# Kernel tuning notes

Measured on AMD Instinct MI355X. Metric: run time of the kernel, lower is better.

The kernel has to match this reference:

```python
import jax, jax.numpy as jnp
import numpy as np

N, C, H, W = 8, 128, 56, 56
CO = C // 8  # 16


def setup_inputs() -> dict:
    key = jax.random.key(0)
    k1, k2, k3, k4 = jax.random.split(key, 4)
    x = jax.random.normal(k1, (N, C, H, W), dtype=jnp.float32)
    # p_3: Conv2d(c*35 -> c//8, 1x1). The unfold channel order is (c, kh=5, kw=7),
    # so the 1x1 conv over c*35 channels is exactly a dilated 5x7 conv with
    # weight [CO, C, 5, 7] and rhs_dilation (2, 3).
    w3 = jax.random.normal(k2, (CO, C, 5, 7), dtype=jnp.float32) * 0.02
    w4 = jax.random.normal(k3, (CO, CO), dtype=jnp.float32) * 0.1
    w5 = jax.random.normal(k4, (C, CO), dtype=jnp.float32) * 0.1
    return {"x": x, "w3": w3, "w4": w4, "w5": w5}


def reference(x, w3, w4, w5):
    # Fused equivalent of: unfold(5x1, dil 2, pad 4) -> unfold(1x7, dil 3, pad 9)
    # -> 1x1 conv (c*35 -> c//8). Padding (4,4)/(9,9) keeps 'same' spatial size.
    y = jax.lax.conv_general_dilated(
        x, w3,
        window_strides=(1, 1),
        padding=((4, 4), (9, 9)),
        rhs_dilation=(2, 3),
        dimension_numbers=("NCHW", "OIHW", "NCHW"),
    )  # [N, CO, H, W]
    y = jnp.einsum("oc,nchw->nohw", w4, y)  # p_4: 1x1 conv CO->CO
    y = jnp.einsum("oc,nchw->nohw", w5, y)  # p_5: 1x1 conv CO->C
    return y
```

## Files before the change

### kernel.cpp

```cpp
#include <hip/hip_runtime.h>

#define BN 8
#define BC 128
#define BH 56
#define BW 56
#define HW 3136
#define NTAP 35
#define WS_WC 71680
#define WS_XP (WS_WC + 4096)
#define XROW 2368
#define XS_OFF 0
#define Y3_OFF 15360
#define WA_OFF 17920
#define SMEM_SZ 53760

typedef unsigned short u16;
typedef unsigned int u32;
typedef __bf16 bf16x8 __attribute__((ext_vector_type(8)));
typedef float f32x4 __attribute__((ext_vector_type(4)));

__device__ __forceinline__ u16 f2b(float f) {
    unsigned u = __float_as_uint(f);
    return (u16)((u + 0x7FFFu + ((u >> 16) & 1u)) >> 16);
}
__device__ __forceinline__ u32 pack2(float a, float b) {
    return (u32)f2b(a) | ((u32)f2b(b) << 16);
}
__device__ __forceinline__ void dma16(const void* g, void* l) {
    __builtin_amdgcn_global_load_lds(
        (const __attribute__((address_space(1))) u32*)g,
        (__attribute__((address_space(3))) u32*)l, 16, 0, 0);
}

__global__ __launch_bounds__(256) void prep_all(
    const float* __restrict__ x, const float* __restrict__ w3,
    const float* __restrict__ w4, const float* __restrict__ w5,
    u16* __restrict__ ws)
{
    const int b = blockIdx.x;
    const int tid = threadIdx.x;

    if (b >= 2048) {
        int i = (b - 2048) * 256 + tid;
        if (i < WS_WC) {
            int j = i & 7, lane = (i >> 3) & 63, r = i >> 9;
            int tap = r % NTAP, cc = r / NTAP;
            int q = lane >> 4, lm = lane & 15;
            ws[i] = f2b(w3[(lm * BC + cc * 32 + q * 8 + j) * NTAP + tap]);
        } else if (i < WS_WC + 4096) {
            int i2 = i - WS_WC;
            int j = i2 & 7, lane = (i2 >> 3) & 63, ot = i2 >> 9;
            int q = lane >> 4, lm = lane & 15, o = ot * 16 + lm, k = q * 8 + j;
            float s = 0.f;
            if (k < 16)
                for (int c = 0; c < 16; ++c) s += w5[o * 16 + c] * w4[c * 16 + k];
            ws[i] = f2b(s);
        }
        return;
    }

    __shared__ float ls[32][57];
    const int hp = b & 63, cc = (b >> 6) & 3, n = b >> 8;
    u32* dst = (u32*)(ws + WS_XP + (size_t)((n * 4 + cc) * 64 + hp) * XROW);
    const int gr = hp - 4;

    if ((unsigned)gr >= BH) {
        for (int i = tid; i < XROW / 2; i += 256) dst[i] = 0u;
        return;
    }
    for (int i = tid; i < 32 * 14; i += 256) {
        int c = i / 14, w4i = i % 14;
        float4 v = *(const float4*)(x + ((size_t)(n * BC + cc * 32 + c) * BH + gr) * BW + 4 * w4i);
        ls[c][4 * w4i + 0] = v.x;
        ls[c][4 * w4i + 1] = v.y;
        ls[c][4 * w4i + 2] = v.z;
        ls[c][4 * w4i + 3] = v.w;
    }
    __syncthreads();
    for (int i = tid; i < 74 * 16; i += 256) {
        int col = i >> 4, cp = i & 15;
        int gw = col - 9;
        u32 v = 0u;
        if ((unsigned)gw < BW) v = pack2(ls[2 * cp][gw], ls[2 * cp + 1][gw]);
        dst[col * 16 + cp] = v;
    }
}

__global__ __launch_bounds__(512, 6) void conv_mfma(
    const u16* __restrict__ wsT, float* __restrict__ out)
{
    __shared__ __align__(16) char smem[SMEM_SZ];
    u16* xs  = (u16*)(smem + XS_OFF);
    u16* y3T = (u16*)(smem + Y3_OFF);
    u16* wA  = (u16*)(smem + WA_OFF);
    float* cbuf = (float*)(smem + XS_OFF);

    const int n = blockIdx.x & 7;
    const int r0 = blockIdx.x >> 3;
    const int h = r0 >> 1, wh = r0 & 1;
    const int tid = threadIdx.x, lane = tid & 63, wv = tid >> 6;
    const int wt = wv >> 2, g = wv & 3;
    const int q = lane >> 4, lm = lane & 15;
    const int wl = wt * 16 + lm;
    const int wg = wh * 28 + wl;
    const bool wok = (wl < 28);

    if (tid < 256) ((u32*)(y3T + (tid >> 3) * 40))[8 + (tid & 7)] = 0u;

    f32x4 acc = {0.f, 0.f, 0.f, 0.f};
    const int t0 = 9 * g;
    const int ntap = (g == 3) ? 8 : 9;

    for (int cc = 0; cc < 4; ++cc) {
        __syncthreads();

        const u16* xbase = wsT + WS_XP + (size_t)((n * 4 + cc) * 64 + h) * XROW
                         + wh * 28 * 32;
        for (int k = wv; k < 15; k += 8) {
            int r = k / 3, s = k - 3 * r;
            dma16(xbase + (size_t)(2 * r) * XROW + s * 512 + lane * 8,
                  smem + XS_OFF + r * 3072 + s * 1024 + lane * 16);
        }
        const u16* wbase = wsT + (size_t)cc * NTAP * 512;
        for (int k = wv; k < NTAP; k += 8)
            dma16(wbase + (size_t)k * 512 + lane * 8,
                  smem + WA_OFF + k * 1024 + lane * 16);

        __syncthreads();

        #pragma unroll
        for (int tt = 0; tt < 9; ++tt) {
            if (tt < ntap) {
                int t = t0 + tt;
                int kh = t / 7, kw = t - 7 * kh;
                bf16x8 a = *(const bf16x8*)(wA + (size_t)(t * 64 + lane) * 8);
                bf16x8 b = *(const bf16x8*)(xs + ((kh * 48 + wl + 3 * kw) * 32 + q * 8));
                acc = __builtin_amdgcn_mfma_f32_16x16x32_bf16(a, b, acc, 0, 0, 0);
            }
        }
    }

    __syncthreads();
    if (g > 0) {
        float* cb = cbuf + ((wt * 3 + (g - 1)) * 64 + lane) * 4;
        cb[0] = acc[0]; cb[1] = acc[1]; cb[2] = acc[2]; cb[3] = acc[3];
    }
    __syncthreads();
    if (g == 0) {
        #pragma unroll
        for (int p = 0; p < 3; ++p) {
            const float* cb = cbuf + ((wt * 3 + p) * 64 + lane) * 4;
            acc[0] += cb[0]; acc[1] += cb[1]; acc[2] += cb[2]; acc[3] += cb[3];
        }
        u32 lo = wok ? pack2(acc[0], acc[1]) : 0u;
        u32 hi = wok ? pack2(acc[2], acc[3]) : 0u;
        *(u32*)(y3T + wl * 40 + q * 4)     = lo;
        *(u32*)(y3T + wl * 40 + q * 4 + 2) = hi;
    }
    __syncthreads();

    bf16x8 bfrag = *(const bf16x8*)(y3T + wl * 40 + q * 8);
    #pragma unroll
    for (int i = 0; i < 2; ++i) {
        const int ot = 2 * g + i;
        bf16x8 afrag = *(const bf16x8*)(wsT + WS_WC + (size_t)(ot * 64 + lane) * 8);
        f32x4 c2 = {0.f, 0.f, 0.f, 0.f};
        c2 = __builtin_amdgcn_mfma_f32_16x16x32_bf16(afrag, bfrag, c2, 0, 0, 0);
        if (wok) {
            int o = ot * 16 + q * 4;
            float* po = out + ((size_t)(n * BC + o) * BH + h) * BW + wg;
            po[0]      = c2[0];
            po[HW]     = c2[1];
            po[2 * HW] = c2[2];
            po[3 * HW] = c2[3];
        }
    }
}

extern "C" void kernel_launch(void* const* d_in, const int* in_sizes, int n_in,
                              void* d_out, int out_size, void* d_ws, size_t ws_size,
                              hipStream_t stream)
{
    (void)in_sizes; (void)n_in; (void)out_size; (void)ws_size;
    const float* x  = (const float*)d_in[0];
    const float* w3 = (const float*)d_in[1];
    const float* w4 = (const float*)d_in[2];
    const float* w5 = (const float*)d_in[3];
    u16* ws = (u16*)d_ws;

    prep_all<<<2048 + 296, 256, 0, stream>>>(x, w3, w4, w5, ws);
    conv_mfma<<<BN * BH * 2, 512, 0, stream>>>(ws, (float*)d_out);
}
```

Measured before the change: 90.36 us.

## Process full output rows per block with double-buffered LDS staging

Each block now covers a full 56-wide output row instead of half a row, and each wave computes two column tiles that share one weight fragment. Input and weight staging for the next channel chunk is double-buffered in LDS, so the DMA overlaps the MFMA work and only one barrier per chunk remains. The LDS footprint grows to about 125 KB and launch bounds drop to 2 blocks per CU. This halves the grid to 448 blocks and risks lower occupancy and poorer load balance across CUs.

Measured after the change: 92.19 us. 2.0% more time.

```diff
diff --git a/kernel.cpp b/kernel.cpp
--- a/kernel.cpp
+++ b/kernel.cpp
@@ -9,10 +9,6 @@
 #define WS_WC 71680
 #define WS_XP (WS_WC + 4096)
 #define XROW 2368
-#define XS_OFF 0
-#define Y3_OFF 15360
-#define WA_OFF 17920
-#define SMEM_SZ 53760
 
 typedef unsigned short u16;
 typedef unsigned int u32;
@@ -86,95 +82,119 @@
     }
 }
 
-__global__ __launch_bounds__(512, 6) void conv_mfma(
+#define XSBUF 25600
+#define WABUF 35840
+#define XS_OFF 0
+#define WA_OFF 51200
+#define Y3_OFF 122880
+#define SMEM_SZ 128000
+
+__global__ __launch_bounds__(512, 2) void conv_mfma(
     const u16* __restrict__ wsT, float* __restrict__ out)
 {
     __shared__ __align__(16) char smem[SMEM_SZ];
-    u16* xs  = (u16*)(smem + XS_OFF);
     u16* y3T = (u16*)(smem + Y3_OFF);
-    u16* wA  = (u16*)(smem + WA_OFF);
     float* cbuf = (float*)(smem + XS_OFF);
 
     const int n = blockIdx.x & 7;
-    const int r0 = blockIdx.x >> 3;
-    const int h = r0 >> 1, wh = r0 & 1;
+    const int h = blockIdx.x >> 3;
     const int tid = threadIdx.x, lane = tid & 63, wv = tid >> 6;
-    const int wt = wv >> 2, g = wv & 3;
+    const int g = wv & 3, wp = wv >> 2;
     const int q = lane >> 4, lm = lane & 15;
-    const int wl = wt * 16 + lm;
-    const int wg = wh * 28 + wl;
-    const bool wok = (wl < 28);
-
-    if (tid < 256) ((u32*)(y3T + (tid >> 3) * 40))[8 + (tid & 7)] = 0u;
-
-    f32x4 acc = {0.f, 0.f, 0.f, 0.f};
+    const int c0 = wp * 32 + lm;
+    const int c1 = c0 + 16;
     const int t0 = 9 * g;
     const int ntap = (g == 3) ? 8 : 9;
 
+#define STAGE(CC, BUF) do {                                                   \
+        const u16* xbase = wsT + WS_XP + (size_t)((n * 4 + (CC)) * 64 + h) * XROW; \
+        const u16* wbase = wsT + (size_t)(CC) * NTAP * 512;                   \
+        char* xd = smem + XS_OFF + (BUF) * XSBUF;                             \
+        char* wd = smem + WA_OFF + (BUF) * WABUF;                             \
+        for (int k = wv; k < 60; k += 8) {                                    \
+            if (k < 25) {                                                     \
+                int r = k / 5, s = k - 5 * r;                                 \
+                dma16(xbase + (size_t)(2 * r) * XROW + s * 512 + lane * 8,    \
+                      xd + r * 5120 + s * 1024 + lane * 16);                  \
+            } else {                                                          \
+                int k2 = k - 25;                                              \
+                dma16(wbase + (size_t)k2 * 512 + lane * 8,                    \
+                      wd + (size_t)k2 * 1024 + lane * 16);                    \
+            }                                                                 \
+        }                                                                     \
+    } while (0)
+
+    f32x4 acc0 = {0.f, 0.f, 0.f, 0.f};
+    f32x4 acc1 = {0.f, 0.f, 0.f, 0.f};
+
+    STAGE(0, 0);
+    ((u32*)(y3T + (tid >> 3) * 40))[8 + (tid & 7)] = 0u;
+    __syncthreads();
+
+    #pragma unroll
     for (int cc = 0; cc < 4; ++cc) {
-        __syncthreads();
-
-        const u16* xbase = wsT + WS_XP + (size_t)((n * 4 + cc) * 64 + h) * XROW
-                         + wh * 28 * 32;
-        for (int k = wv; k < 15; k += 8) {
-            int r = k / 3, s = k - 3 * r;
-            dma16(xbase + (size_t)(2 * r) * XROW + s * 512 + lane * 8,
-                  smem + XS_OFF + r * 3072 + s * 1024 + lane * 16);
-        }
-        const u16* wbase = wsT + (size_t)cc * NTAP * 512;
-        for (int k = wv; k < NTAP; k += 8)
-            dma16(wbase + (size_t)k * 512 + lane * 8,
-                  smem + WA_OFF + k * 1024 + lane * 16);
-
-        __syncthreads();
-
+        const int buf = cc & 1;
+        if (cc < 3) STAGE(cc + 1, buf ^ 1);
+        const u16* xsb = (const u16*)(smem + XS_OFF + buf * XSBUF);
+        const u16* wAb = (const u16*)(smem + WA_OFF + buf * WABUF);
         #pragma unroll
         for (int tt = 0; tt < 9; ++tt) {
             if (tt < ntap) {
-                int t = t0 + tt;
-                int kh = t / 7, kw = t - 7 * kh;
-                bf16x8 a = *(const bf16x8*)(wA + (size_t)(t * 64 + lane) * 8);
-                bf16x8 b = *(const bf16x8*)(xs + ((kh * 48 + wl + 3 * kw) * 32 + q * 8));
-                acc = __builtin_amdgcn_mfma_f32_16x16x32_bf16(a, b, acc, 0, 0, 0);
+                const int t = t0 + tt;
+                const int kh = t / 7, kw = t - 7 * kh;
+                bf16x8 a = *(const bf16x8*)(wAb + (size_t)(t * 64 + lane) * 8);
+                const u16* xrow = xsb + (size_t)(kh * 80 + 3 * kw) * 32 + q * 8;
+                bf16x8 b0 = *(const bf16x8*)(xrow + (size_t)c0 * 32);
+                acc0 = __builtin_amdgcn_mfma_f32_16x16x32_bf16(a, b0, acc0, 0, 0, 0);
+                bf16x8 b1 = *(const bf16x8*)(xrow + (size_t)c1 * 32);
+                acc1 = __builtin_amdgcn_mfma_f32_16x16x32_bf16(a, b1, acc1, 0, 0, 0);
             }
         }
-    }
-
-    __syncthreads();
+        if (cc < 3) __syncthreads();
+    }
+
     if (g > 0) {
-        float* cb = cbuf + ((wt * 3 + (g - 1)) * 64 + lane) * 4;
-        cb[0] = acc[0]; cb[1] = acc[1]; cb[2] = acc[2]; cb[3] = acc[3];
+        float* cb = cbuf + (size_t)(((wp * 3 + (g - 1)) * 2) * 64 + lane) * 4;
+        *(f32x4*)cb = acc0;
+        *(f32x4*)(cb + 256) = acc1;
     }
     __syncthreads();
     if (g == 0) {
         #pragma unroll
         for (int p = 0; p < 3; ++p) {
-            const float* cb = cbuf + ((wt * 3 + p) * 64 + lane) * 4;
-            acc[0] += cb[0]; acc[1] += cb[1]; acc[2] += cb[2]; acc[3] += cb[3];
-        }
-        u32 lo = wok ? pack2(acc[0], acc[1]) : 0u;
-        u32 hi = wok ? pack2(acc[2], acc[3]) : 0u;
-        *(u32*)(y3T + wl * 40 + q * 4)     = lo;
-        *(u32*)(y3T + wl * 40 + q * 4 + 2) = hi;
-    }
-    __syncthreads();
-
-    bf16x8 bfrag = *(const bf16x8*)(y3T + wl * 40 + q * 8);
+            const float* cb = cbuf + (size_t)(((wp * 3 + p) * 2) * 64 + lane) * 4;
+            f32x4 v0 = *(const f32x4*)cb;
+            f32x4 v1 = *(const f32x4*)(cb + 256);
+            acc0[0] += v0[0]; acc0[1] += v0[1]; acc0[2] += v0[2]; acc0[3] += v0[3];
+            acc1[0] += v1[0]; acc1[1] += v1[1]; acc1[2] += v1[2]; acc1[3] += v1[3];
+        }
+        const bool ok1 = (c1 < BW);
+        *(u32*)(y3T + c0 * 40 + q * 4)     = pack2(acc0[0], acc0[1]);
+        *(u32*)(y3T + c0 * 40 + q * 4 + 2) = pack2(acc0[2], acc0[3]);
+        *(u32*)(y3T + c1 * 40 + q * 4)     = ok1 ? pack2(acc1[0], acc1[1]) : 0u;
+        *(u32*)(y3T + c1 * 40 + q * 4 + 2) = ok1 ? pack2(acc1[2], acc1[3]) : 0u;
+    }
+    __syncthreads();
+
+    const int ct = wv & 3, og = wv >> 2;
+    const int wgc = ct * 16 + lm;
+    bf16x8 bfrag = *(const bf16x8*)(y3T + (size_t)wgc * 40 + q * 8);
     #pragma unroll
-    for (int i = 0; i < 2; ++i) {
-        const int ot = 2 * g + i;
+    for (int i = 0; i < 4; ++i) {
+        const int ot = 4 * og + i;
         bf16x8 afrag = *(const bf16x8*)(wsT + WS_WC + (size_t)(ot * 64 + lane) * 8);
         f32x4 c2 = {0.f, 0.f, 0.f, 0.f};
         c2 = __builtin_amdgcn_mfma_f32_16x16x32_bf16(afrag, bfrag, c2, 0, 0, 0);
-        if (wok) {
-            int o = ot * 16 + q * 4;
-            float* po = out + ((size_t)(n * BC + o) * BH + h) * BW + wg;
+        if (wgc < BW) {
+            const int o = ot * 16 + q * 4;
+            float* po = out + ((size_t)(n * BC + o) * BH + h) * BW + wgc;
             po[0]      = c2[0];
             po[HW]     = c2[1];
             po[2 * HW] = c2[2];
             po[3 * HW] = c2[3];
         }
     }
+#undef STAGE
 }
 
 extern "C" void kernel_launch(void* const* d_in, const int* in_sizes, int n_in,
@@ -189,5 +209,5 @@
     u16* ws = (u16*)d_ws;
 
     prep_all<<<2048 + 296, 256, 0, stream>>>(x, w3, w4, w5, ws);
-    conv_mfma<<<BN * BH * 2, 512, 0, stream>>>(ws, (float*)d_out);
-}
+    conv_mfma<<<BN * BH, 512, 0, stream>>>(ws, (float*)d_out);
+}
```
